# Performance work log

Measured on AMD Instinct MI355X. Metric: run time of the kernel, lower is better.

Reference implementation:

```python
import jax, jax.numpy as jnp
import numpy as np

V, E, H, L = 10000, 512, 512, 3   # vocab, embed dim, hidden, num decoder layers
SOS, EOS = 1, 2


def setup_inputs() -> dict:
    key = jax.random.key(0)
    ks = jax.random.split(key, 16)
    N, To, Ti = 32, 64, 512
    s = 0.05
    inp = {
        'padded_input': jax.random.randint(ks[0], (N, To), 0, V),
        'encoder_padded_outputs': jax.random.normal(ks[1], (N, Ti, H), jnp.float32),
        'emb': jax.random.normal(ks[2], (V, E), jnp.float32) * s,
        # layer 0 LSTMCell: input = embed + encoder context (E + H)
        'W_ih0': jax.random.normal(ks[3], (4 * H, E + H), jnp.float32) * s,
        'W_hh0': jax.random.normal(ks[4], (4 * H, H), jnp.float32) * s,
        'b_ih0': jnp.zeros((4 * H,), jnp.float32),
        'b_hh0': jnp.zeros((4 * H,), jnp.float32),
        # layers 1..L-1 LSTMCells (stacked)
        'W_ih_r': jax.random.normal(ks[5], (L - 1, 4 * H, H), jnp.float32) * s,
        'W_hh_r': jax.random.normal(ks[6], (L - 1, 4 * H, H), jnp.float32) * s,
        'b_ih_r': jnp.zeros((L - 1, 4 * H), jnp.float32),
        'b_hh_r': jnp.zeros((L - 1, 4 * H), jnp.float32),
        # MLP: Linear(2H -> H), Tanh, Linear(H -> V)
        'W1': jax.random.normal(ks[7], (H, 2 * H), jnp.float32) * s,
        'b1': jnp.zeros((H,), jnp.float32),
        'W2': jax.random.normal(ks[8], (V, H), jnp.float32) * s,
        'b2': jnp.zeros((V,), jnp.float32),
    }
    return inp


def _lstm_cell(x, h, c, Wi, Wh, bi, bh):
    # torch.nn.LSTMCell gate order: i, f, g, o
    g = x @ Wi.T + h @ Wh.T + bi + bh
    i, f, gg, o = jnp.split(g, 4, axis=-1)
    c2 = jax.nn.sigmoid(f) * c + jax.nn.sigmoid(i) * jnp.tanh(gg)
    h2 = jax.nn.sigmoid(o) * jnp.tanh(c2)
    return h2, c2


def reference(padded_input, encoder_padded_outputs, emb,
              W_ih0, W_hh0, b_ih0, b_hh0,
              W_ih_r, W_hh_r, b_ih_r, b_hh_r,
              W1, b1, W2, b2):
    N, To = padded_input.shape
    sos = jnp.full((N, 1), SOS, padded_input.dtype)
    eos = jnp.full((N, 1), EOS, padded_input.dtype)
    ys_in = jnp.concatenate([sos, padded_input], axis=1)    # [N, T]
    ys_out = jnp.concatenate([padded_input, eos], axis=1)   # [N, T]
    xs = jnp.transpose(emb[ys_in], (1, 0, 2))               # [T, N, E]

    def step(carry, x_t):
        h, c, att_c = carry                                  # h,c: [L,N,H]; att_c: [N,H]
        rnn_in = jnp.concatenate([x_t, att_c], axis=1)       # [N, E+H]
        h0, c0 = _lstm_cell(rnn_in, h[0], c[0], W_ih0, W_hh0, b_ih0, b_hh0)
        hs, cs = [h0], [c0]
        for l in range(L - 1):
            hl, cl = _lstm_cell(hs[-1], h[l + 1], c[l + 1],
                                W_ih_r[l], W_hh_r[l], b_ih_r[l], b_hh_r[l])
            hs.append(hl); cs.append(cl)
        r = hs[-1]                                           # [N, H]
        scores = jnp.einsum('nh,nth->nt', r, encoder_padded_outputs)
        w = jax.nn.softmax(scores, axis=-1)
        att = jnp.einsum('nt,nth->nh', w, encoder_padded_outputs)
        mlp_in = jnp.concatenate([r, att], axis=1)           # [N, 2H]
        y = jnp.tanh(mlp_in @ W1.T + b1) @ W2.T + b2         # [N, V]
        return (jnp.stack(hs), jnp.stack(cs), att), y

    h0 = jnp.zeros((L, N, H), encoder_padded_outputs.dtype)
    c0 = jnp.zeros((L, N, H), encoder_padded_outputs.dtype)
    a0 = jnp.zeros((N, H), encoder_padded_outputs.dtype)
    _, ys = jax.lax.scan(step, (h0, c0, a0), xs)             # [T, N, V]
    y_all = jnp.transpose(ys, (1, 0, 2))                     # [N, T, V]

    logp = jax.nn.log_softmax(y_all, axis=-1)
    nll = -jnp.take_along_axis(logp, ys_out[..., None], axis=-1)[..., 0]
    ce_loss = nll.mean()
    return y_all, ce_loss
```

## Files before the change

kernel.cpp:

```cpp
#include <hip/hip_runtime.h>
#include <hip/hip_bf16.h>
#include <hip/hip_fp16.h>

#define NB 32
#define TO 64
#define TT 65
#define TI 512
#define VV 10000
#define HH 512
#define G4 2048
#define SOS_ID 1
#define EOS_ID 2
#define NBLK 256
#define GBLK 32

typedef unsigned uvec4 __attribute__((ext_vector_type(4)));
typedef unsigned uvec2 __attribute__((ext_vector_type(2)));
typedef _Float16 h2v __attribute__((ext_vector_type(2)));

__device__ __forceinline__ float cload1(const float* p) {
    unsigned v = __hip_atomic_load((const unsigned*)p,
                                   __ATOMIC_RELAXED, __HIP_MEMORY_SCOPE_AGENT);
    return __uint_as_float(v);
}
__device__ __forceinline__ float2 cload2(const float* p) {
    unsigned long long v = __hip_atomic_load((const unsigned long long*)p,
                                             __ATOMIC_RELAXED, __HIP_MEMORY_SCOPE_AGENT);
    float2 r;
    r.x = __uint_as_float((unsigned)(v & 0xffffffffull));
    r.y = __uint_as_float((unsigned)(v >> 32));
    return r;
}
__device__ __forceinline__ void cstore(float* p, float v) {
    __hip_atomic_store((unsigned*)p, __float_as_uint(v),
                       __ATOMIC_RELAXED, __HIP_MEMORY_SCOPE_AGENT);
}

__device__ __forceinline__ void gbar(int* flags, int g, int s, int& epoch) {
    asm volatile("s_waitcnt vmcnt(0) lgkmcnt(0)" ::: "memory");
    __syncthreads();
    epoch++;
    int tid = threadIdx.x;
    if (tid == 0)
        __hip_atomic_store(&flags[(g * 32 + s) * 16], epoch,
                           __ATOMIC_RELAXED, __HIP_MEMORY_SCOPE_AGENT);
    if (tid < 32) {
        for (;;) {
            int v = __hip_atomic_load(&flags[(g * 32 + tid) * 16],
                                      __ATOMIC_RELAXED, __HIP_MEMORY_SCOPE_AGENT);
            unsigned long long b = __ballot(v >= epoch);
            if ((b & 0xffffffffull) == 0xffffffffull) break;
            __builtin_amdgcn_s_sleep(1);
        }
    }
    __syncthreads();
}

__device__ __forceinline__ float bf2f(unsigned u16) {
    return __uint_as_float(u16 << 16);
}
__device__ __forceinline__ unsigned f2bf(float f) {
    unsigned u = __float_as_uint(f);
    return (u + 0x7fffu + ((u >> 16) & 1u)) >> 16;
}
__device__ __forceinline__ unsigned packh2(float a, float b) {
    __half2 h = __floats2half2_rn(a, b);
    return *(unsigned*)&h;
}
__device__ __forceinline__ h2v uash2(unsigned u) {
    union { unsigned u; h2v h; } c; c.u = u; return c.h;
}

template <int KQ4>
__device__ __forceinline__ void lstm_phase(
    const unsigned* __restrict__ Wtb, const float* __restrict__ bi,
    const float* __restrict__ bh, float* __restrict__ hout,
    float& creg, float* __restrict__ mlprow,
    const float4* xs4, float* sg, int s, int n0, int gn, int gml, int gm) {
    int tid = threadIdx.x;
    int lane = tid & 63, wv = tid >> 6;
    const uvec2* wp = (const uvec2*)Wtb + (long)(wv * KQ4) * 2048 + (s * 64 + lane);
    const float4* xp = xs4 + wv * KQ4 * 4;
    float a0 = 0.f, a1 = 0.f, a2 = 0.f, a3 = 0.f;
#pragma unroll 4
    for (int kq = 0; kq < KQ4; kq++) {
        uvec2 u = wp[(long)kq * 2048];
        float w0 = bf2f(u.x & 0xffffu), w1 = bf2f(u.x >> 16);
        float w2 = bf2f(u.y & 0xffffu), w3 = bf2f(u.y >> 16);
        float4 x0 = xp[4 * kq], x1 = xp[4 * kq + 1];
        float4 x2 = xp[4 * kq + 2], x3 = xp[4 * kq + 3];
        a0 = fmaf(w0, x0.x, a0); a1 = fmaf(w0, x0.y, a1);
        a2 = fmaf(w0, x0.z, a2); a3 = fmaf(w0, x0.w, a3);
        a0 = fmaf(w1, x1.x, a0); a1 = fmaf(w1, x1.y, a1);
        a2 = fmaf(w1, x1.z, a2); a3 = fmaf(w1, x1.w, a3);
        a0 = fmaf(w2, x2.x, a0); a1 = fmaf(w2, x2.y, a1);
        a2 = fmaf(w2, x2.z, a2); a3 = fmaf(w2, x2.w, a3);
        a0 = fmaf(w3, x3.x, a0); a1 = fmaf(w3, x3.y, a1);
        a2 = fmaf(w3, x3.z, a2); a3 = fmaf(w3, x3.w, a3);
    }
    float4 r4; r4.x = a0; r4.y = a1; r4.z = a2; r4.w = a3;
    ((float4*)sg)[wv * 64 + lane] = r4;
    __syncthreads();
    if (tid < 64) {
        float ga[4];
#pragma unroll
        for (int q = 0; q < 4; q++) {
            int c = q * 16 + gml;
            float sum = 0.f;
#pragma unroll
            for (int w = 0; w < 16; w++) sum += sg[(w * 64 + c) * 4 + gn];
            ga[q] = sum;
        }
        float gi = ga[0] + bi[gm] + bh[gm];
        float gf = ga[1] + bi[512 + gm] + bh[512 + gm];
        float gg = ga[2] + bi[1024 + gm] + bh[1024 + gm];
        float go = ga[3] + bi[1536 + gm] + bh[1536 + gm];
        float si = 1.f / (1.f + expf(-gi));
        float sf = 1.f / (1.f + expf(-gf));
        float so = 1.f / (1.f + expf(-go));
        float c2 = sf * creg + si * tanhf(gg);
        creg = c2;
        float hv = so * tanhf(c2);
        cstore(&hout[(n0 + gn) * 512 + gm], hv);
        if (mlprow) mlprow[(long)(n0 + gn) * 1024 + gm] = hv;
    }
}

__global__ __launch_bounds__(1024, 4) void decode_loop(
    const unsigned* __restrict__ Wtb0, const unsigned* __restrict__ Wtb1,
    const unsigned* __restrict__ Wtb2, const float* __restrict__ emb,
    const int* __restrict__ tokens, const float* __restrict__ enc,
    const float* __restrict__ b_ih0, const float* __restrict__ b_hh0,
    const float* __restrict__ b_ih_r, const float* __restrict__ b_hh_r,
    float* __restrict__ hbuf, float* __restrict__ attc,
    float* __restrict__ scor, float* __restrict__ mlpin, int* flags) {
    __shared__ float4 xs4[1536];
    __shared__ float sg[4096];
    __shared__ unsigned short enct[32768];
    float* xsf = (float*)xs4;

    int tid = threadIdx.x, b = blockIdx.x;
    int g = b >> 5, s = b & 31;
    int epoch = 0;
    int n0 = g * 4;
    int lane = tid & 63;
    int gn = tid >> 4, gml = tid & 15;
    int gm = s * 16 + gml;
    int na = n0 + (s >> 3), tiq = s & 7;
    float c0r = 0.f, c1r = 0.f, c2r = 0.f;

    {
        int tl = tid >> 4;
        int gb = (tid & 15) * 4;
        const float* ebase = enc + ((long)na * TI + tiq * 64 + tl) * HH;
#pragma unroll
        for (int q = 0; q < 4; q++) {
            int gg = gb + q;
            const float* ep = ebase + gg * 8;
            float4 lo = *(const float4*)ep;
            float4 hi = *(const float4*)(ep + 4);
            uvec4 pk;
            pk.x = f2bf(lo.x) | (f2bf(lo.y) << 16);
            pk.y = f2bf(lo.z) | (f2bf(lo.w) << 16);
            pk.z = f2bf(hi.x) | (f2bf(hi.y) << 16);
            pk.w = f2bf(hi.z) | (f2bf(hi.w) << 16);
            *(uvec4*)(enct + tl * 512 + (gg ^ (tl & 7)) * 8) = pk;
        }
    }
    __syncthreads();

    for (int t = 0; t < TT; t++) {
        int rp = t & 1;
        float* hOld = hbuf + rp * 3 * NB * HH;
        float* hNew = hbuf + (rp ^ 1) * 3 * NB * HH;
        float* h0r = hOld;
        float* h1r = hOld + NB * HH;
        float* h2r = hOld + 2 * NB * HH;
        float* h0w = hNew;
        float* h1w = hNew + NB * HH;
        float* h2w = hNew + 2 * NB * HH;

        if (tid < 768) {
            int r0 = (t == 0) ? SOS_ID : tokens[(n0 + 0) * TO + t - 1];
            int r1 = (t == 0) ? SOS_ID : tokens[(n0 + 1) * TO + t - 1];
            int r2 = (t == 0) ? SOS_ID : tokens[(n0 + 2) * TO + t - 1];
            int r3 = (t == 0) ? SOS_ID : tokens[(n0 + 3) * TO + t - 1];
            int k = tid * 2;
            float2 va, vb, vc, vd;
            if (k < 512) {
                va = *(const float2*)(emb + (long)r0 * 512 + k);
                vb = *(const float2*)(emb + (long)r1 * 512 + k);
                vc = *(const float2*)(emb + (long)r2 * 512 + k);
                vd = *(const float2*)(emb + (long)r3 * 512 + k);
            } else if (k < 1024) {
                int kk = k - 512;
                va = cload2(attc + (n0 + 0) * 512 + kk);
                vb = cload2(attc + (n0 + 1) * 512 + kk);
                vc = cload2(attc + (n0 + 2) * 512 + kk);
                vd = cload2(attc + (n0 + 3) * 512 + kk);
                if (t && ((kk >> 4) == s)) {
                    float* mp = mlpin + ((long)(t - 1) * NB + n0) * 1024 + 512 + kk;
                    mp[0] = va.x; mp[1] = va.y;
                    mp[1024] = vb.x; mp[1025] = vb.y;
                    mp[2048] = vc.x; mp[2049] = vc.y;
                    mp[3072] = vd.x; mp[3073] = vd.y;
                }
            } else {
                int kk = k - 1024;
                va = cload2(h0r + (n0 + 0) * 512 + kk);
                vb = cload2(h0r + (n0 + 1) * 512 + kk);
                vc = cload2(h0r + (n0 + 2) * 512 + kk);
                vd = cload2(h0r + (n0 + 3) * 512 + kk);
            }
            float4 x0, x1;
            x0.x = va.x; x0.y = vb.x; x0.z = vc.x; x0.w = vd.x;
            x1.x = va.y; x1.y = vb.y; x1.z = vc.y; x1.w = vd.y;
            xs4[k] = x0; xs4[k + 1] = x1;
        }
        __syncthreads();
        lstm_phase<24>(Wtb0, b_ih0, b_hh0, h0w, c0r, nullptr,
                       xs4, sg, s, n0, gn, gml, gm);
        gbar(flags, g, s, epoch);

        if (tid < 64) cstore(&attc[n0 * 512 + s * 64 + tid], 0.f);
        if (tid < 512) {
            int k = tid * 2;
            const float* base = (k < 512) ? h0w : (h1r - 512);
            float2 va = cload2(base + (n0 + 0) * 512 + k);
            float2 vb = cload2(base + (n0 + 1) * 512 + k);
            float2 vc = cload2(base + (n0 + 2) * 512 + k);
            float2 vd = cload2(base + (n0 + 3) * 512 + k);
            float4 x0, x1;
            x0.x = va.x; x0.y = vb.x; x0.z = vc.x; x0.w = vd.x;
            x1.x = va.y; x1.y = vb.y; x1.z = vc.y; x1.w = vd.y;
            xs4[k] = x0; xs4[k + 1] = x1;
        }
        __syncthreads();
        lstm_phase<16>(Wtb1, b_ih_r, b_hh_r, h1w, c1r, nullptr,
                       xs4, sg, s, n0, gn, gml, gm);
        gbar(flags, g, s, epoch);

        if (tid < 512) {
            int k = tid * 2;
            const float* base = (k < 512) ? h1w : (h2r - 512);
            float2 va = cload2(base + (n0 + 0) * 512 + k);
            float2 vb = cload2(base + (n0 + 1) * 512 + k);
            float2 vc = cload2(base + (n0 + 2) * 512 + k);
            float2 vd = cload2(base + (n0 + 3) * 512 + k);
            float4 x0, x1;
            x0.x = va.x; x0.y = vb.x; x0.z = vc.x; x0.w = vd.x;
            x1.x = va.y; x1.y = vb.y; x1.z = vc.y; x1.w = vd.y;
            xs4[k] = x0; xs4[k + 1] = x1;
        }
        __syncthreads();
        lstm_phase<16>(Wtb2, b_ih_r + G4, b_hh_r + G4, h2w, c2r,
                       mlpin + (long)t * NB * 1024,
                       xs4, sg, s, n0, gn, gml, gm);
        gbar(flags, g, s, epoch);

        if (tid < 512) xsf[tid] = cload1(h2w + na * 512 + tid);
        __syncthreads();
        {
            int tl = tid & 63, kh = tid >> 6;
            float acc = 0.f;
#pragma unroll
            for (int q = 0; q < 4; q++) {
                int gg = kh * 4 + q;
                uvec4 e = *(const uvec4*)(enct + tl * 512 + ((gg ^ (tl & 7)) * 8));
                const float* hp = xsf + gg * 8;
                acc += bf2f(e.x & 0xffffu) * hp[0] + bf2f(e.x >> 16) * hp[1]
                     + bf2f(e.y & 0xffffu) * hp[2] + bf2f(e.y >> 16) * hp[3]
                     + bf2f(e.z & 0xffffu) * hp[4] + bf2f(e.z >> 16) * hp[5]
                     + bf2f(e.w & 0xffffu) * hp[6] + bf2f(e.w >> 16) * hp[7];
            }
            sg[tid] = acc;
            __syncthreads();
            if (tid < 64) {
                float sv = 0.f;
#pragma unroll
                for (int w = 0; w < 16; w++) sv += sg[tid + 64 * w];
                cstore(&scor[na * 512 + tiq * 64 + tid], sv);
            }
        }
        gbar(flags, g, s, epoch);

        {
            float sv = (tid < 512) ? cload1(scor + na * 512 + tid) : -1e30f;
            int wv = tid >> 6;
            float m = sv;
#pragma unroll
            for (int o = 32; o > 0; o >>= 1) m = fmaxf(m, __shfl_xor(m, o));
            if (lane == 0) sg[wv] = m;
            __syncthreads();
            m = sg[0];
#pragma unroll
            for (int w = 1; w < 16; w++) m = fmaxf(m, sg[w]);
            float e = expf(sv - m);
            float ss = e;
#pragma unroll
            for (int o = 32; o > 0; o >>= 1) ss += __shfl_xor(ss, o);
            if (lane == 0) sg[32 + wv] = ss;
            __syncthreads();
            float tot = 0.f;
#pragma unroll
            for (int w = 0; w < 16; w++) tot += sg[32 + w];
            float inv = 1.f / tot;
            __syncthreads();
            if (tid < 512) xsf[tid] = e * inv;
            __syncthreads();

            int hp = (tid & 255) * 2, tis = (tid >> 8) * 16;
            int gb2 = hp >> 3, wrd = hp & 7;
            const float* wrow = xsf + tiq * 64;
            float a0 = 0.f, a1 = 0.f;
#pragma unroll 8
            for (int q = 0; q < 16; q++) {
                int tl = tis + q;
                unsigned u = *(const unsigned*)(enct + tl * 512 +
                                                ((gb2 ^ (tl & 7)) * 8) + wrd);
                float w = wrow[tl];
                a0 = fmaf(w, bf2f(u & 0xffffu), a0);
                a1 = fmaf(w, bf2f(u >> 16), a1);
            }
            float* prt = xsf + 1024;
            prt[(tid >> 8) * 512 + hp] = a0;
            prt[(tid >> 8) * 512 + hp + 1] = a1;
            __syncthreads();
            if (tid < 512) {
                int h = tid;
                float v = prt[h] + prt[512 + h] + prt[1024 + h] + prt[1536 + h];
                atomicAdd(&attc[na * 512 + h], v);
            }
        }
        gbar(flags, g, s, epoch);
    }

    if (tid < 64) {
        int h = tiq * 64 + tid;
        mlpin[((long)(TT - 1) * NB + na) * 1024 + 512 + h] =
            cload1(attc + na * 512 + h);
    }
}

__global__ void transpose_lstm_q(const float* __restrict__ Wih, int KA,
                                 const float* __restrict__ Whh,
                                 unsigned* __restrict__ Wtb) {
    int K = KA + 512;
    long total = (long)(K / 4) * 4096;
    for (long idx = (long)blockIdx.x * 256 + threadIdx.x; idx < total;
         idx += (long)gridDim.x * 256) {
        int c2 = (int)(idx % 4096);
        int kq = (int)(idx / 4096);
        int c = c2 >> 1, half = c2 & 1;
        int sI = c >> 6, r = c & 63, gg = r >> 4, ml = r & 15;
        int j = gg * 512 + sI * 16 + ml;
        int k0 = kq * 4 + half * 2, k1 = k0 + 1;
        float w0 = (k0 < KA) ? Wih[(long)j * KA + k0] : Whh[(long)j * 512 + (k0 - KA)];
        float w1 = (k1 < KA) ? Wih[(long)j * KA + k1] : Whh[(long)j * 512 + (k1 - KA)];
        Wtb[idx] = f2bf(w0) | (f2bf(w1) << 16);
    }
}

__global__ void transpose_w2_h2(const float* __restrict__ W2,
                                unsigned* __restrict__ Wh) {
    long total = (long)256 * 10240;
    for (long idx = (long)blockIdx.x * 256 + threadIdx.x; idx < total;
         idx += (long)gridDim.x * 256) {
        int j = (int)(idx % 10240);
        int kk = (int)(idx / 10240);
        float lo = 0.f, hi = 0.f;
        if (j < VV) {
            lo = W2[(long)j * 512 + 2 * kk];
            hi = W2[(long)j * 512 + 2 * kk + 1];
        }
        Wh[idx] = packh2(lo, hi);
    }
}

__global__ void transpose_cat(const float* __restrict__ A, int KA,
                              int J, int Jp, float* __restrict__ Wt) {
    long total = (long)KA * Jp;
    for (long idx = (long)blockIdx.x * 256 + threadIdx.x; idx < total;
         idx += (long)gridDim.x * 256) {
        int j = (int)(idx % Jp);
        int k = (int)(idx / Jp);
        Wt[idx] = (j < J) ? A[(long)j * KA + k] : 0.f;
    }
}

__global__ void gemm_mlp1(const float* __restrict__ Wt,
                          const float* __restrict__ X,
                          const float* __restrict__ bias,
                          unsigned* __restrict__ outh) {
    __shared__ float xs[64 * 12];
    int m0 = blockIdx.x * 8;
    int lane = threadIdx.x & 63;
    int wv = threadIdx.x >> 6;
    int jp = wv * 64 + lane;
    float acc0[8], acc1[8];
#pragma unroll
    for (int q = 0; q < 8; q++) { acc0[q] = 0.f; acc1[q] = 0.f; }
    for (int kc = 0; kc < 1024; kc += 64) {
        __syncthreads();
        for (int idx = threadIdx.x; idx < 512; idx += 256) {
            int k = idx >> 3, n = idx & 7;
            xs[k * 12 + n] = X[(long)(m0 + n) * 1024 + kc + k];
        }
        __syncthreads();
        const float2* wpp = (const float2*)(Wt + (long)kc * 512) + jp;
#pragma unroll 4
        for (int k = 0; k < 64; k++) {
            float2 w = wpp[(long)k * 256];
            const float4* xv = (const float4*)(xs + k * 12);
            float4 x0 = xv[0], x1 = xv[1];
            acc0[0] += w.x * x0.x; acc0[1] += w.x * x0.y;
            acc0[2] += w.x * x0.z; acc0[3] += w.x * x0.w;
            acc0[4] += w.x * x1.x; acc0[5] += w.x * x1.y;
            acc0[6] += w.x * x1.z; acc0[7] += w.x * x1.w;
            acc1[0] += w.y * x0.x; acc1[1] += w.y * x0.y;
            acc1[2] += w.y * x0.z; acc1[3] += w.y * x0.w;
            acc1[4] += w.y * x1.x; acc1[5] += w.y * x1.y;
            acc1[6] += w.y * x1.z; acc1[7] += w.y * x1.w;
        }
    }
    float b0 = bias[2 * jp], b1 = bias[2 * jp + 1];
#pragma unroll
    for (int n = 0; n < 8; n++) {
        float v0 = tanhf(acc0[n] + b0);
        float v1 = tanhf(acc1[n] + b1);
        outh[(long)(m0 + n) * 256 + jp] = packh2(v0, v1);
    }
}

__global__ void gemm_mlp2(const unsigned* __restrict__ Wh,
                          const unsigned* __restrict__ Xh,
                          const float* __restrict__ bias,
                          float* __restrict__ out) {
    __shared__ unsigned xs[256 * 36];
    int t = blockIdx.y;
    int m0 = t * 32;
    int lane = threadIdx.x & 63;
    int wv = threadIdx.x >> 6;
    int j0 = blockIdx.x * 256 + wv * 64 + lane;
    float acc0[32], acc1[32];
#pragma unroll
    for (int q = 0; q < 32; q++) { acc0[q] = 0.f; acc1[q] = 0.f; }
    for (int idx = threadIdx.x; idx < 8192; idx += 256) {
        int kk = idx & 255, n = idx >> 8;
        xs[kk * 36 + n] = Xh[(long)(m0 + n) * 256 + kk];
    }
    __syncthreads();
    const unsigned* wpp = Wh + j0;
#pragma unroll 2
    for (int kk = 0; kk < 256; kk++) {
        unsigned u0 = wpp[(long)kk * 10240];
        unsigned u1 = wpp[(long)kk * 10240 + 5120];
        h2v w0 = uash2(u0), w1 = uash2(u1);
        const uvec4* xv = (const uvec4*)(xs + kk * 36);
#pragma unroll
        for (int q = 0; q < 8; q++) {
            uvec4 x4 = xv[q];
            acc0[4 * q + 0] = __builtin_amdgcn_fdot2(uash2(x4.x), w0, acc0[4 * q + 0], false);
            acc0[4 * q + 1] = __builtin_amdgcn_fdot2(uash2(x4.y), w0, acc0[4 * q + 1], false);
            acc0[4 * q + 2] = __builtin_amdgcn_fdot2(uash2(x4.z), w0, acc0[4 * q + 2], false);
            acc0[4 * q + 3] = __builtin_amdgcn_fdot2(uash2(x4.w), w0, acc0[4 * q + 3], false);
            acc1[4 * q + 0] = __builtin_amdgcn_fdot2(uash2(x4.x), w1, acc1[4 * q + 0], false);
            acc1[4 * q + 1] = __builtin_amdgcn_fdot2(uash2(x4.y), w1, acc1[4 * q + 1], false);
            acc1[4 * q + 2] = __builtin_amdgcn_fdot2(uash2(x4.z), w1, acc1[4 * q + 2], false);
            acc1[4 * q + 3] = __builtin_amdgcn_fdot2(uash2(x4.w), w1, acc1[4 * q + 3], false);
        }
    }
#pragma unroll
    for (int nn = 0; nn < 32; nn++) {
        long row = (long)nn * TT + t;
        float* po = out + row * VV;
        int ja = j0, jb = j0 + 5120;
        po[ja] = acc0[nn] + bias[ja];
        if (jb < VV) po[jb] = acc1[nn] + bias[jb];
    }
}

__global__ void loss_rows(const float* __restrict__ out, const int* __restrict__ tokens,
                          float* __restrict__ nll) {
    __shared__ float red[256];
    int row = blockIdx.x;
    int n = row / TT, t = row % TT;
    const float* y = out + (long)row * VV;
    int tid = threadIdx.x;
    float m = -1e30f;
    for (int v = tid; v < VV; v += 256) m = fmaxf(m, y[v]);
    red[tid] = m;
    __syncthreads();
    for (int s = 128; s > 0; s >>= 1) {
        if (tid < s) red[tid] = fmaxf(red[tid], red[tid + s]);
        __syncthreads();
    }
    m = red[0];
    __syncthreads();
    float sum = 0.f;
    for (int v = tid; v < VV; v += 256) sum += expf(y[v] - m);
    red[tid] = sum;
    __syncthreads();
    for (int s = 128; s > 0; s >>= 1) {
        if (tid < s) red[tid] += red[tid + s];
        __syncthreads();
    }
    if (tid == 0) {
        int target = (t < TO) ? tokens[n * TO + t] : EOS_ID;
        nll[row] = m + logf(red[0]) - y[target];
    }
}

__global__ void loss_final(const float* __restrict__ nll, float* __restrict__ out_loss) {
    __shared__ float red[256];
    int tid = threadIdx.x;
    float s = 0.f;
    for (int i = tid; i < NB * TT; i += 256) s += nll[i];
    red[tid] = s;
    __syncthreads();
    for (int k = 128; k > 0; k >>= 1) {
        if (tid < k) red[tid] += red[tid + k];
        __syncthreads();
    }
    if (tid == 0) *out_loss = red[0] / (float)(NB * TT);
}

extern "C" void kernel_launch(void* const* d_in, const int* in_sizes, int n_in,
                              void* d_out, int out_size, void* d_ws, size_t ws_size,
                              hipStream_t stream) {
    const int* padded   = (const int*)d_in[0];
    const float* enc    = (const float*)d_in[1];
    const float* emb    = (const float*)d_in[2];
    const float* W_ih0  = (const float*)d_in[3];
    const float* W_hh0  = (const float*)d_in[4];
    const float* b_ih0  = (const float*)d_in[5];
    const float* b_hh0  = (const float*)d_in[6];
    const float* W_ih_r = (const float*)d_in[7];
    const float* W_hh_r = (const float*)d_in[8];
    const float* b_ih_r = (const float*)d_in[9];
    const float* b_hh_r = (const float*)d_in[10];
    const float* W1     = (const float*)d_in[11];
    const float* b1     = (const float*)d_in[12];
    const float* W2     = (const float*)d_in[13];
    const float* b2     = (const float*)d_in[14];
    float* out = (float*)d_out;
    float* ws  = (float*)d_ws;

    unsigned* Wtb0 = (unsigned*)ws;
    unsigned* Wtb1 = Wtb0 + 384 * 4096;
    unsigned* Wtb2 = Wtb1 + 256 * 4096;
    unsigned* Wh   = Wtb2 + 256 * 4096;
    float* Wm1  = (float*)(Wh + 256 * 10240);
    float* hbuf = Wm1 + 1024 * 512;
    float* attc = hbuf + 2 * 3 * NB * HH;
    float* scor = attc + NB * HH;
    float* mlpin= scor + NB * TI;
    unsigned* y1h = (unsigned*)(mlpin + (long)TT * NB * 1024);
    float* nll  = (float*)(y1h + (long)TT * NB * 256);
    int*   flags= (int*)(nll + 2080);

    hipMemsetAsync(hbuf, 0, (size_t)(2 * 3 * NB * HH + 2 * NB * HH) * sizeof(float), stream);
    hipMemsetAsync(flags, 0, 8 * 32 * 16 * sizeof(int), stream);

    transpose_cat<<<1024, 256, 0, stream>>>(W1, 1024, 512, 512, Wm1);
    transpose_lstm_q<<<2048, 256, 0, stream>>>(W_ih0, 1024, W_hh0, Wtb0);
    transpose_lstm_q<<<2048, 256, 0, stream>>>(W_ih_r, 512, W_hh_r, Wtb1);
    transpose_lstm_q<<<2048, 256, 0, stream>>>(W_ih_r + 2048 * 512, 512,
                                               W_hh_r + 2048 * 512, Wtb2);
    transpose_w2_h2<<<2048, 256, 0, stream>>>(W2, Wh);

    decode_loop<<<NBLK, 1024, 0, stream>>>(Wtb0, Wtb1, Wtb2, emb, padded, enc,
                                           b_ih0, b_hh0, b_ih_r, b_hh_r,
                                           hbuf, attc, scor, mlpin, flags);

    gemm_mlp1<<<260, 256, 0, stream>>>(Wm1, mlpin, b1, y1h);
    gemm_mlp2<<<dim3(20, TT), 256, 0, stream>>>(Wh, y1h, b2, out);
    loss_rows<<<NB * TT, 256, 0, stream>>>(out, padded, nll);
    loss_final<<<1, 256, 0, stream>>>(nll, out + (long)NB * TT * VV);
}
```

Before: 2.417 ms.

## Prefetch recurrent inputs off the critical path and parallelize gate reduction

The LSTM gate reduction now runs in two stages: every thread first sums four of the sixteen wave partials, then 64 threads finish the reduction, replacing a 16-term serial loop per gate. Staging of inputs that are already available (the previous-step h of the next layer, plus the next step's embedding and layer-0 hidden state) moves into idle threads during the gate epilogue and the attention phase. Only the value produced by the preceding layer is loaded after each grid barrier, which shortens the serial chain between barriers. Attention scratch moves into the sg buffer so the prefetched xs4 contents survive, at the cost of an extra 4KB of shared memory and an extra __syncthreads per LSTM phase.

```diff
diff --git a/kernel.cpp b/kernel.cpp
--- a/kernel.cpp
+++ b/kernel.cpp
@@ -12,7 +12,6 @@
 #define SOS_ID 1
 #define EOS_ID 2
 #define NBLK 256
-#define GBLK 32
 
 typedef unsigned uvec4 __attribute__((ext_vector_type(4)));
 typedef unsigned uvec2 __attribute__((ext_vector_type(2)));
@@ -76,11 +75,12 @@
     const unsigned* __restrict__ Wtb, const float* __restrict__ bi,
     const float* __restrict__ bh, float* __restrict__ hout,
     float& creg, float* __restrict__ mlprow,
-    const float4* xs4, float* sg, int s, int n0, int gn, int gml, int gm) {
+    float4* xs4, float* sg, float* sg2, int s, int n0,
+    const float* __restrict__ pre) {
     int tid = threadIdx.x;
     int lane = tid & 63, wv = tid >> 6;
     const uvec2* wp = (const uvec2*)Wtb + (long)(wv * KQ4) * 2048 + (s * 64 + lane);
-    const float4* xp = xs4 + wv * KQ4 * 4;
+    const float4* xp = (const float4*)xs4 + wv * KQ4 * 4;
     float a0 = 0.f, a1 = 0.f, a2 = 0.f, a3 = 0.f;
 #pragma unroll 4
     for (int kq = 0; kq < KQ4; kq++) {
@@ -101,15 +101,23 @@
     float4 r4; r4.x = a0; r4.y = a1; r4.z = a2; r4.w = a3;
     ((float4*)sg)[wv * 64 + lane] = r4;
     __syncthreads();
+    {
+        int c = tid >> 4, n = (tid >> 2) & 3, w4 = tid & 3;
+        float sum = sg[((w4 * 4 + 0) * 64 + c) * 4 + n]
+                  + sg[((w4 * 4 + 1) * 64 + c) * 4 + n]
+                  + sg[((w4 * 4 + 2) * 64 + c) * 4 + n]
+                  + sg[((w4 * 4 + 3) * 64 + c) * 4 + n];
+        sg2[tid] = sum;
+    }
+    __syncthreads();
     if (tid < 64) {
+        int gn = tid >> 4, gml = tid & 15, gm = s * 16 + gml;
         float ga[4];
 #pragma unroll
         for (int q = 0; q < 4; q++) {
             int c = q * 16 + gml;
-            float sum = 0.f;
-#pragma unroll
-            for (int w = 0; w < 16; w++) sum += sg[(w * 64 + c) * 4 + gn];
-            ga[q] = sum;
+            const float* p = sg2 + c * 16 + gn * 4;
+            ga[q] = p[0] + p[1] + p[2] + p[3];
         }
         float gi = ga[0] + bi[gm] + bh[gm];
         float gf = ga[1] + bi[512 + gm] + bh[512 + gm];
@@ -123,6 +131,16 @@
         float hv = so * tanhf(c2);
         cstore(&hout[(n0 + gn) * 512 + gm], hv);
         if (mlprow) mlprow[(long)(n0 + gn) * 1024 + gm] = hv;
+    } else if (pre && tid >= 512 && tid < 768) {
+        int k = 512 + (tid - 512) * 2;
+        float2 va = cload2(pre + (n0 + 0) * 512 + (k - 512));
+        float2 vb = cload2(pre + (n0 + 1) * 512 + (k - 512));
+        float2 vc = cload2(pre + (n0 + 2) * 512 + (k - 512));
+        float2 vd = cload2(pre + (n0 + 3) * 512 + (k - 512));
+        float4 x0, x1;
+        x0.x = va.x; x0.y = vb.x; x0.z = vc.x; x0.w = vd.x;
+        x1.x = va.y; x1.y = vb.y; x1.z = vc.y; x1.w = vd.y;
+        xs4[k] = x0; xs4[k + 1] = x1;
     }
 }
 
@@ -136,6 +154,7 @@
     float* __restrict__ scor, float* __restrict__ mlpin, int* flags) {
     __shared__ float4 xs4[1536];
     __shared__ float sg[4096];
+    __shared__ float sg2[1024];
     __shared__ unsigned short enct[32768];
     float* xsf = (float*)xs4;
 
@@ -144,8 +163,6 @@
     int epoch = 0;
     int n0 = g * 4;
     int lane = tid & 63;
-    int gn = tid >> 4, gml = tid & 15;
-    int gm = s * 16 + gml;
     int na = n0 + (s >> 3), tiq = s & 7;
     float c0r = 0.f, c1r = 0.f, c2r = 0.f;
 
@@ -180,82 +197,84 @@
         float* h1w = hNew + NB * HH;
         float* h2w = hNew + 2 * NB * HH;
 
-        if (tid < 768) {
-            int r0 = (t == 0) ? SOS_ID : tokens[(n0 + 0) * TO + t - 1];
-            int r1 = (t == 0) ? SOS_ID : tokens[(n0 + 1) * TO + t - 1];
-            int r2 = (t == 0) ? SOS_ID : tokens[(n0 + 2) * TO + t - 1];
-            int r3 = (t == 0) ? SOS_ID : tokens[(n0 + 3) * TO + t - 1];
-            int k = tid * 2;
-            float2 va, vb, vc, vd;
-            if (k < 512) {
-                va = *(const float2*)(emb + (long)r0 * 512 + k);
-                vb = *(const float2*)(emb + (long)r1 * 512 + k);
-                vc = *(const float2*)(emb + (long)r2 * 512 + k);
-                vd = *(const float2*)(emb + (long)r3 * 512 + k);
-            } else if (k < 1024) {
-                int kk = k - 512;
-                va = cload2(attc + (n0 + 0) * 512 + kk);
-                vb = cload2(attc + (n0 + 1) * 512 + kk);
-                vc = cload2(attc + (n0 + 2) * 512 + kk);
-                vd = cload2(attc + (n0 + 3) * 512 + kk);
-                if (t && ((kk >> 4) == s)) {
+        if (t == 0) {
+            if (tid < 768) {
+                int k = tid * 2;
+                float2 va, vb, vc, vd;
+                if (k < 512) {
+                    va = *(const float2*)(emb + (long)SOS_ID * 512 + k);
+                    vb = va; vc = va; vd = va;
+                } else if (k < 1024) {
+                    va.x = va.y = 0.f; vb = va; vc = va; vd = va;
+                } else {
+                    int kk = k - 1024;
+                    va = cload2(h0r + (n0 + 0) * 512 + kk);
+                    vb = cload2(h0r + (n0 + 1) * 512 + kk);
+                    vc = cload2(h0r + (n0 + 2) * 512 + kk);
+                    vd = cload2(h0r + (n0 + 3) * 512 + kk);
+                }
+                float4 x0, x1;
+                x0.x = va.x; x0.y = vb.x; x0.z = vc.x; x0.w = vd.x;
+                x1.x = va.y; x1.y = vb.y; x1.z = vc.y; x1.w = vd.y;
+                xs4[k] = x0; xs4[k + 1] = x1;
+            }
+        } else {
+            if (tid < 256) {
+                int kk = tid * 2;
+                float2 va = cload2(attc + (n0 + 0) * 512 + kk);
+                float2 vb = cload2(attc + (n0 + 1) * 512 + kk);
+                float2 vc = cload2(attc + (n0 + 2) * 512 + kk);
+                float2 vd = cload2(attc + (n0 + 3) * 512 + kk);
+                if ((kk >> 4) == s) {
                     float* mp = mlpin + ((long)(t - 1) * NB + n0) * 1024 + 512 + kk;
                     mp[0] = va.x; mp[1] = va.y;
                     mp[1024] = vb.x; mp[1025] = vb.y;
                     mp[2048] = vc.x; mp[2049] = vc.y;
                     mp[3072] = vd.x; mp[3073] = vd.y;
                 }
-            } else {
-                int kk = k - 1024;
-                va = cload2(h0r + (n0 + 0) * 512 + kk);
-                vb = cload2(h0r + (n0 + 1) * 512 + kk);
-                vc = cload2(h0r + (n0 + 2) * 512 + kk);
-                vd = cload2(h0r + (n0 + 3) * 512 + kk);
+                float4 x0, x1;
+                x0.x = va.x; x0.y = vb.x; x0.z = vc.x; x0.w = vd.x;
+                x1.x = va.y; x1.y = vb.y; x1.z = vc.y; x1.w = vd.y;
+                xs4[512 + kk] = x0; xs4[512 + kk + 1] = x1;
             }
+        }
+        __syncthreads();
+        lstm_phase<24>(Wtb0, b_ih0, b_hh0, h0w, c0r, nullptr,
+                       xs4, sg, sg2, s, n0, h1r);
+        gbar(flags, g, s, epoch);
+
+        if (tid < 64) cstore(&attc[n0 * 512 + s * 64 + tid], 0.f);
+        if (tid < 256) {
+            int k = tid * 2;
+            float2 va = cload2(h0w + (n0 + 0) * 512 + k);
+            float2 vb = cload2(h0w + (n0 + 1) * 512 + k);
+            float2 vc = cload2(h0w + (n0 + 2) * 512 + k);
+            float2 vd = cload2(h0w + (n0 + 3) * 512 + k);
             float4 x0, x1;
             x0.x = va.x; x0.y = vb.x; x0.z = vc.x; x0.w = vd.x;
             x1.x = va.y; x1.y = vb.y; x1.z = vc.y; x1.w = vd.y;
             xs4[k] = x0; xs4[k + 1] = x1;
         }
         __syncthreads();
-        lstm_phase<24>(Wtb0, b_ih0, b_hh0, h0w, c0r, nullptr,
-                       xs4, sg, s, n0, gn, gml, gm);
+        lstm_phase<16>(Wtb1, b_ih_r, b_hh_r, h1w, c1r, nullptr,
+                       xs4, sg, sg2, s, n0, h2r);
         gbar(flags, g, s, epoch);
 
-        if (tid < 64) cstore(&attc[n0 * 512 + s * 64 + tid], 0.f);
-        if (tid < 512) {
+        if (tid < 256) {
             int k = tid * 2;
-            const float* base = (k < 512) ? h0w : (h1r - 512);
-            float2 va = cload2(base + (n0 + 0) * 512 + k);
-            float2 vb = cload2(base + (n0 + 1) * 512 + k);
-            float2 vc = cload2(base + (n0 + 2) * 512 + k);
-            float2 vd = cload2(base + (n0 + 3) * 512 + k);
+            float2 va = cload2(h1w + (n0 + 0) * 512 + k);
+            float2 vb = cload2(h1w + (n0 + 1) * 512 + k);
+            float2 vc = cload2(h1w + (n0 + 2) * 512 + k);
+            float2 vd = cload2(h1w + (n0 + 3) * 512 + k);
             float4 x0, x1;
             x0.x = va.x; x0.y = vb.x; x0.z = vc.x; x0.w = vd.x;
             x1.x = va.y; x1.y = vb.y; x1.z = vc.y; x1.w = vd.y;
             xs4[k] = x0; xs4[k + 1] = x1;
         }
         __syncthreads();
-        lstm_phase<16>(Wtb1, b_ih_r, b_hh_r, h1w, c1r, nullptr,
-                       xs4, sg, s, n0, gn, gml, gm);
-        gbar(flags, g, s, epoch);
-
-        if (tid < 512) {
-            int k = tid * 2;
-            const float* base = (k < 512) ? h1w : (h2r - 512);
-            float2 va = cload2(base + (n0 + 0) * 512 + k);
-            float2 vb = cload2(base + (n0 + 1) * 512 + k);
-            float2 vc = cload2(base + (n0 + 2) * 512 + k);
-            float2 vd = cload2(base + (n0 + 3) * 512 + k);
-            float4 x0, x1;
-            x0.x = va.x; x0.y = vb.x; x0.z = vc.x; x0.w = vd.x;
-            x1.x = va.y; x1.y = vb.y; x1.z = vc.y; x1.w = vd.y;
-            xs4[k] = x0; xs4[k + 1] = x1;
-        }
-        __syncthreads();
         lstm_phase<16>(Wtb2, b_ih_r + G4, b_hh_r + G4, h2w, c2r,
                        mlpin + (long)t * NB * 1024,
-                       xs4, sg, s, n0, gn, gml, gm);
+                       xs4, sg, sg2, s, n0, nullptr);
         gbar(flags, g, s, epoch);
 
         if (tid < 512) xsf[tid] = cload1(h2w + na * 512 + tid);
@@ -306,12 +325,12 @@
             for (int w = 0; w < 16; w++) tot += sg[32 + w];
             float inv = 1.f / tot;
             __syncthreads();
-            if (tid < 512) xsf[tid] = e * inv;
+            if (tid < 512) sg[64 + tid] = e * inv;
             __syncthreads();
 
             int hp = (tid & 255) * 2, tis = (tid >> 8) * 16;
             int gb2 = hp >> 3, wrd = hp & 7;
-            const float* wrow = xsf + tiq * 64;
+            const float* wrow = sg + 64 + tiq * 64;
             float a0 = 0.f, a1 = 0.f;
 #pragma unroll 8
             for (int q = 0; q < 16; q++) {
@@ -322,7 +341,7 @@
                 a0 = fmaf(w, bf2f(u & 0xffffu), a0);
                 a1 = fmaf(w, bf2f(u >> 16), a1);
             }
-            float* prt = xsf + 1024;
+            float* prt = sg + 1024;
             prt[(tid >> 8) * 512 + hp] = a0;
             prt[(tid >> 8) * 512 + hp + 1] = a1;
             __syncthreads();
@@ -330,6 +349,29 @@
                 int h = tid;
                 float v = prt[h] + prt[512 + h] + prt[1024 + h] + prt[1536 + h];
                 atomicAdd(&attc[na * 512 + h], v);
+            }
+            if (t + 1 < TT) {
+                if (tid < 512) {
+                    int k = tid;
+                    int r0 = tokens[(n0 + 0) * TO + t];
+                    int r1 = tokens[(n0 + 1) * TO + t];
+                    int r2 = tokens[(n0 + 2) * TO + t];
+                    int r3 = tokens[(n0 + 3) * TO + t];
+                    float4 v;
+                    v.x = emb[(long)r0 * 512 + k];
+                    v.y = emb[(long)r1 * 512 + k];
+                    v.z = emb[(long)r2 * 512 + k];
+                    v.w = emb[(long)r3 * 512 + k];
+                    xs4[k] = v;
+                } else {
+                    int k = tid - 512;
+                    float4 v;
+                    v.x = cload1(h0w + (n0 + 0) * 512 + k);
+                    v.y = cload1(h0w + (n0 + 1) * 512 + k);
+                    v.z = cload1(h0w + (n0 + 2) * 512 + k);
+                    v.w = cload1(h0w + (n0 + 3) * 512 + k);
+                    xs4[1024 + k] = v;
+                }
             }
         }
         gbar(flags, g, s, epoch);
```

New measurement: 2.330 ms. 1.04x faster.
